# Kernel optimization log

Measured on AMD Instinct MI355X. Metric: run time of the kernel, lower is better.

## Reference

```python
import jax, jax.numpy as jnp
import numpy as np

N_NODES = 50000
N_EDGES = 1000000
IN_DIM, HID_DIM, OUT_DIM = 128, 64, 16


def setup_inputs() -> dict:
    key = jax.random.key(0)
    k1, k2, k3, k4 = jax.random.split(key, 4)
    x = jax.random.normal(k1, (N_NODES, IN_DIM), dtype=jnp.float32)
    edge_index = jax.random.randint(k2, (2, N_EDGES), 0, N_NODES, dtype=jnp.int64)
    # Glorot-style scaling for weights, zero bias (PyG GCNConv default init style)
    W1 = jax.random.normal(k3, (IN_DIM, HID_DIM), dtype=jnp.float32) * (1.0 / np.sqrt(IN_DIM))
    b1 = jnp.zeros((HID_DIM,), dtype=jnp.float32)
    W2 = jax.random.normal(k4, (HID_DIM, OUT_DIM), dtype=jnp.float32) * (1.0 / np.sqrt(HID_DIM))
    b2 = jnp.zeros((OUT_DIM,), dtype=jnp.float32)
    return {"x": x, "edge_index": edge_index, "W1": W1, "b1": b1, "W2": W2, "b2": b2}


def gcn_conv(x, src, dst, W, b, num_nodes):
    """PyG GCNConv: add self loops, symmetric deg^{-1/2} normalization,
    linear transform, gather-scale-scatter aggregation, bias."""
    # degree includes self loops (src/dst already augmented by caller)
    deg = jax.ops.segment_sum(jnp.ones_like(dst, dtype=x.dtype), dst, num_segments=num_nodes)
    dinv = jnp.where(deg > 0, deg ** -0.5, 0.0)
    norm = dinv[src] * dinv[dst]            # [E']
    h = x @ W                                # [N, F_out] transform before aggregation
    msg = h[src] * norm[:, None]             # gather + scale
    out = jax.ops.segment_sum(msg, dst, num_segments=num_nodes)  # scatter-add
    return out + b


def reference(x, edge_index, W1, b1, W2, b2):
    n = x.shape[0]
    loops = jnp.arange(n, dtype=edge_index.dtype)
    src = jnp.concatenate([edge_index[0], loops])
    dst = jnp.concatenate([edge_index[1], loops])
    h = gcn_conv(x, src, dst, W1, b1, n)
    h = jax.nn.relu(h)
    out = gcn_conv(h, src, dst, W2, b2, n)
    return out
```

## Files before the change

kernel.cpp:

```cpp
#include <hip/hip_runtime.h>
#include <hip/hip_bf16.h>

#define IN_DIM 128
#define HID_DIM 64
#define OUT_DIM 16

#define SSHIFT 7
#define SMASK 127
#define CHUNK 4096
#define CBLK 256

static __device__ __forceinline__ unsigned short f2bf(float f) {
    unsigned u = __float_as_uint(f);
    unsigned r = u + 0x7fffu + ((u >> 16) & 1u);
    return (unsigned short)(r >> 16);
}
static __device__ __forceinline__ unsigned packbf2(float a, float b) {
    return (unsigned)f2bf(a) | ((unsigned)f2bf(b) << 16);
}
static __device__ __forceinline__ float bflo(unsigned v) { return __uint_as_float(v << 16); }
static __device__ __forceinline__ float bfhi(unsigned v) { return __uint_as_float(v & 0xffff0000u); }

__global__ __launch_bounds__(CBLK) void passA(const int* __restrict__ dst,
                                              int* __restrict__ cm,
                                              int E, int NS, int NSP) {
    __shared__ int cnt[512];
    int t = threadIdx.x;
    for (int s = t; s < NS; s += CBLK) cnt[s] = 0;
    __syncthreads();
    int base = blockIdx.x * CHUNK;
    #pragma unroll 4
    for (int k = 0; k < CHUNK; k += CBLK) {
        int i = base + k + t;
        if (i < E) atomicAdd(&cnt[dst[i] >> SSHIFT], 1);
    }
    __syncthreads();
    for (int s = t; s < NS; s += CBLK) cm[blockIdx.x * NSP + s] = cnt[s];
}

__global__ __launch_bounds__(256) void passB1(int* __restrict__ cm, int* __restrict__ tot,
                                              int B, int NSP) {
    __shared__ int sv[256];
    int t = threadIdx.x, s = blockIdx.x;
    int v = (t < B) ? cm[t * NSP + s] : 0;
    sv[t] = v;
    __syncthreads();
    for (int off = 1; off < 256; off <<= 1) {
        int tmp = (t >= off) ? sv[t - off] : 0;
        __syncthreads();
        sv[t] += tmp;
        __syncthreads();
    }
    if (t < B) cm[t * NSP + s] = sv[t] - v;
    if (t == 255) tot[s] = sv[255];
}

__global__ __launch_bounds__(CBLK) void passC(const int* __restrict__ src,
                                              const int* __restrict__ dst,
                                              const int* __restrict__ cm,
                                              const int* __restrict__ tot,
                                              int* __restrict__ eb,
                                              int E, int NS, int NSP) {
    __shared__ int sb[512];
    __shared__ int cur[512];
    int t = threadIdx.x, b = blockIdx.x;
    int i0 = t, i1 = t + 256;
    int v0 = (i0 < NS) ? tot[i0] : 0;
    int v1 = (i1 < NS) ? tot[i1] : 0;
    sb[i0] = v0; sb[i1] = v1;
    __syncthreads();
    for (int off = 1; off < 512; off <<= 1) {
        int t0 = (i0 >= off) ? sb[i0 - off] : 0;
        int t1 = (i1 >= off) ? sb[i1 - off] : 0;
        __syncthreads();
        sb[i0] += t0; sb[i1] += t1;
        __syncthreads();
    }
    if (i0 < NS) cur[i0] = (sb[i0] - v0) + cm[b * NSP + i0];
    if (i1 < NS) cur[i1] = (sb[i1] - v1) + cm[b * NSP + i1];
    __syncthreads();
    int base = b * CHUNK;
    #pragma unroll 4
    for (int k = 0; k < CHUNK; k += CBLK) {
        int i = base + k + t;
        if (i < E) {
            int d = dst[i];
            int s = d >> SSHIFT;
            int pos = atomicAdd(&cur[s], 1);
            eb[pos] = src[i] | ((d & SMASK) << 17);
        }
    }
}

__global__ __launch_bounds__(256) void passD(const int* __restrict__ eb,
                                             const int* __restrict__ tot,
                                             int* __restrict__ csr_src,
                                             int* __restrict__ row_ptr,
                                             float* __restrict__ dinv,
                                             int N, int E, int NS) {
    __shared__ int red[256];
    __shared__ int deg[128], incl[128], cur[128];
    int s = blockIdx.x, t = threadIdx.x;
    if (t < 128) deg[t] = 0;
    int part = 0;
    for (int k = t; k < s; k += 256) part += tot[k];
    red[t] = part;
    __syncthreads();
    for (int off = 128; off >= 1; off >>= 1) {
        if (t < off) red[t] += red[t + off];
        __syncthreads();
    }
    int b0 = red[0];
    int cnt = tot[s];
    for (int k = t; k < cnt; k += 256) atomicAdd(&deg[eb[b0 + k] >> 17], 1);
    __syncthreads();
    if (t < 128) incl[t] = deg[t];
    __syncthreads();
    for (int off = 1; off < 128; off <<= 1) {
        int tmp = 0;
        if (t < 128 && t >= off) tmp = incl[t - off];
        __syncthreads();
        if (t < 128) incl[t] += tmp;
        __syncthreads();
    }
    if (t < 128) {
        int loff = incl[t] - deg[t];
        cur[t] = b0 + loff;
        int n = (s << SSHIFT) + t;
        if (n < N) {
            row_ptr[n] = b0 + loff;
            dinv[n] = rsqrtf((float)(deg[t] + 1));
        }
    }
    if (s == NS - 1 && t == 0) row_ptr[N] = E;
    __syncthreads();
    for (int k = t; k < cnt; k += 256) {
        int v = eb[b0 + k];
        int dl = v >> 17;
        int p = atomicAdd(&cur[dl], 1);
        csr_src[p] = v & 0x1FFFF;
    }
}

__global__ __launch_bounds__(256) void gemm1_kernel(const float* __restrict__ x,
                                                    const float* __restrict__ W1,
                                                    const float* __restrict__ dinv,
                                                    unsigned* __restrict__ h1u, int N) {
    __shared__ __align__(16) float sW[IN_DIM * HID_DIM];
    __shared__ __align__(16) float sx[16 * IN_DIM];
    int t = threadIdx.x;
    int node0 = blockIdx.x * 16;

    const float4* W4  = (const float4*)W1;
    float4*       sW4 = (float4*)sW;
    for (int i = t; i < (IN_DIM * HID_DIM) / 4; i += 256) sW4[i] = W4[i];

    const float4* x4  = (const float4*)x;
    float4*       sx4 = (float4*)sx;
    for (int i = t; i < (16 * IN_DIM) / 4; i += 256) {
        int r = i >> 5, c = i & 31;
        int n = node0 + r; if (n >= N) n = 0;
        sx4[(r << 5) + c] = x4[(size_t)n * 32 + c];
    }
    __syncthreads();

    int ln = t >> 4, jj = t & 15;
    int n = node0 + ln;
    float4 acc = {0.f, 0.f, 0.f, 0.f};
    const float* xr = sx + ln * IN_DIM;
    #pragma unroll 4
    for (int k = 0; k < IN_DIM; ++k) {
        float  xk = xr[k];
        float4 wv = ((const float4*)(sW + k * HID_DIM))[jj];
        acc.x += xk * wv.x; acc.y += xk * wv.y; acc.z += xk * wv.z; acc.w += xk * wv.w;
    }
    if (n <= N) {
        float dn = (n < N) ? dinv[n] : 0.f;
        uint2 pv;
        pv.x = packbf2(acc.x * dn, acc.y * dn);
        pv.y = packbf2(acc.z * dn, acc.w * dn);
        ((uint2*)(h1u + (size_t)n * 32))[jj] = pv;
    }
}

__global__ __launch_bounds__(256) void agg1_kernel(const unsigned* __restrict__ h1u,
                                                   const int* __restrict__ row_ptr,
                                                   const int* __restrict__ csr_src,
                                                   const float* __restrict__ dinv,
                                                   const float* __restrict__ b1,
                                                   unsigned* __restrict__ h1au, int N) {
    int t = threadIdx.x;
    int lane = t & 63;
    int h  = lane >> 5;
    int l  = lane & 31;
    int es = l >> 3;
    int dg = l & 7;
    int n = blockIdx.x * 8 + ((t >> 6) << 1) + h;
    if (n >= N) return;

    int e0 = row_ptr[n], e1 = row_ptr[n + 1];
    const uint4* rb = (const uint4*)h1u;
    int sb = h << 5;

    float a0 = 0.f, a1 = 0.f, a2 = 0.f, a3 = 0.f,
          a4 = 0.f, a5 = 0.f, a6 = 0.f, a7 = 0.f;

    for (int base = e0 - 1; base < e1; base += 32) {
        int idx = base + l;
        int sld = N;
        if (idx == e0 - 1) sld = n;
        else if (idx < e1) sld = csr_src[idx];
        int lim = e1 - base;
        if (lim > 32) lim = 32;
        int nr = (lim + 3) >> 2;
        nr = (nr + 1) & ~1;
        for (int r = 0; r < nr; r += 2) {
            int sA = __shfl(sld, sb + ((r + 0) << 2) + es);
            int sB = __shfl(sld, sb + ((r + 1) << 2) + es);
            uint4 vA = rb[(size_t)sA * 8 + dg];
            uint4 vB = rb[(size_t)sB * 8 + dg];
            a0 += bflo(vA.x) + bflo(vB.x);
            a1 += bfhi(vA.x) + bfhi(vB.x);
            a2 += bflo(vA.y) + bflo(vB.y);
            a3 += bfhi(vA.y) + bfhi(vB.y);
            a4 += bflo(vA.z) + bflo(vB.z);
            a5 += bfhi(vA.z) + bfhi(vB.z);
            a6 += bflo(vA.w) + bflo(vB.w);
            a7 += bfhi(vA.w) + bfhi(vB.w);
        }
    }
    #pragma unroll
    for (int m = 8; m <= 16; m <<= 1) {
        a0 += __shfl_xor(a0, m); a1 += __shfl_xor(a1, m);
        a2 += __shfl_xor(a2, m); a3 += __shfl_xor(a3, m);
        a4 += __shfl_xor(a4, m); a5 += __shfl_xor(a5, m);
        a6 += __shfl_xor(a6, m); a7 += __shfl_xor(a7, m);
    }
    if (es == 0) {
        float dn = dinv[n];
        float4 bA = ((const float4*)b1)[2 * dg];
        float4 bB = ((const float4*)b1)[2 * dg + 1];
        float r0 = fmaxf(fmaf(dn, a0, bA.x), 0.f);
        float r1 = fmaxf(fmaf(dn, a1, bA.y), 0.f);
        float r2 = fmaxf(fmaf(dn, a2, bA.z), 0.f);
        float r3 = fmaxf(fmaf(dn, a3, bA.w), 0.f);
        float r4 = fmaxf(fmaf(dn, a4, bB.x), 0.f);
        float r5 = fmaxf(fmaf(dn, a5, bB.y), 0.f);
        float r6 = fmaxf(fmaf(dn, a6, bB.z), 0.f);
        float r7 = fmaxf(fmaf(dn, a7, bB.w), 0.f);
        uint4 pv;
        pv.x = packbf2(r0, r1); pv.y = packbf2(r2, r3);
        pv.z = packbf2(r4, r5); pv.w = packbf2(r6, r7);
        ((uint4*)h1au)[(size_t)n * 8 + dg] = pv;
    }
}

__global__ __launch_bounds__(256) void gemm2_kernel(const unsigned* __restrict__ h1au,
                                                    const float* __restrict__ W2,
                                                    const float* __restrict__ dinv,
                                                    unsigned* __restrict__ h2u, int N) {
    __shared__ __align__(16) float sW[HID_DIM * OUT_DIM];
    __shared__ __align__(16) float sx[16 * HID_DIM];
    int t = threadIdx.x;
    int node0 = blockIdx.x * 16;

    ((float4*)sW)[t] = ((const float4*)W2)[t];
    for (int i = t; i < 512; i += 256) {
        int r = i >> 5, c = i & 31;
        int n = node0 + r; if (n >= N) n = 0;
        unsigned v = h1au[(size_t)n * 32 + c];
        float2 f; f.x = bflo(v); f.y = bfhi(v);
        *(float2*)(sx + r * HID_DIM + 2 * c) = f;
    }
    __syncthreads();

    int ln = t >> 4, j = t & 15;
    float acc = 0.f;
    const float* xr = sx + ln * HID_DIM;
    #pragma unroll 8
    for (int k = 0; k < HID_DIM; ++k) acc += xr[k] * sW[k * OUT_DIM + j];
    int n = node0 + ln;
    float other = __shfl_xor(acc, 1);
    if (n <= N && (j & 1) == 0) {
        float dn = (n < N) ? dinv[n] : 0.f;
        h2u[(size_t)n * 8 + (j >> 1)] = packbf2(acc * dn, other * dn);
    }
}

__global__ __launch_bounds__(256) void agg2_kernel(const unsigned* __restrict__ h2u,
                                                   const int* __restrict__ row_ptr,
                                                   const int* __restrict__ csr_src,
                                                   const float* __restrict__ dinv,
                                                   const float* __restrict__ b2,
                                                   float* __restrict__ out, int N) {
    int t = threadIdx.x;
    int lane = t & 63;
    int h  = lane >> 4;
    int l  = lane & 15;
    int es = l >> 2;
    int dg = l & 3;
    int n = blockIdx.x * 16 + ((t >> 6) << 2) + h;
    if (n >= N) return;

    int e0 = row_ptr[n], e1 = row_ptr[n + 1];
    const uint2* rb = (const uint2*)h2u;
    int sb = h << 4;

    float a0 = 0.f, a1 = 0.f, a2 = 0.f, a3 = 0.f;

    for (int base = e0 - 1; base < e1; base += 16) {
        int idx = base + l;
        int sld = N;
        if (idx == e0 - 1) sld = n;
        else if (idx < e1) sld = csr_src[idx];
        int lim = e1 - base;
        if (lim > 16) lim = 16;
        int nr = (lim + 3) >> 2;
        nr = (nr + 1) & ~1;
        for (int r = 0; r < nr; r += 2) {
            int sA = __shfl(sld, sb + ((r + 0) << 2) + es);
            int sB = __shfl(sld, sb + ((r + 1) << 2) + es);
            uint2 vA = rb[(size_t)sA * 4 + dg];
            uint2 vB = rb[(size_t)sB * 4 + dg];
            a0 += bflo(vA.x) + bflo(vB.x);
            a1 += bfhi(vA.x) + bfhi(vB.x);
            a2 += bflo(vA.y) + bflo(vB.y);
            a3 += bfhi(vA.y) + bfhi(vB.y);
        }
    }
    #pragma unroll
    for (int m = 4; m <= 8; m <<= 1) {
        a0 += __shfl_xor(a0, m); a1 += __shfl_xor(a1, m);
        a2 += __shfl_xor(a2, m); a3 += __shfl_xor(a3, m);
    }
    if (es == 0) {
        float dn = dinv[n];
        float4 bb = ((const float4*)b2)[dg];
        float4 r;
        r.x = fmaf(dn, a0, bb.x);
        r.y = fmaf(dn, a1, bb.y);
        r.z = fmaf(dn, a2, bb.z);
        r.w = fmaf(dn, a3, bb.w);
        ((float4*)out)[(size_t)n * 4 + dg] = r;
    }
}

extern "C" void kernel_launch(void* const* d_in, const int* in_sizes, int n_in,
                              void* d_out, int out_size, void* d_ws, size_t ws_size,
                              hipStream_t stream) {
    const float* x  = (const float*)d_in[0];
    const int*   ei = (const int*)d_in[1];
    const float* W1 = (const float*)d_in[2];
    const float* b1 = (const float*)d_in[3];
    const float* W2 = (const float*)d_in[4];
    const float* b2 = (const float*)d_in[5];
    float* out = (float*)d_out;

    const int N = in_sizes[0] / IN_DIM;
    const int E = in_sizes[1] / 2;
    const int* src = ei;
    const int* dst = ei + E;

    const int NS  = (N + SMASK) >> SSHIFT;
    const int NSP = NS + 1;
    const int BC  = (E + CHUNK - 1) / CHUNK;

    char* w = (char*)d_ws;
    auto alloc = [&](size_t bytes) -> void* {
        void* p = (void*)w;
        w += (bytes + 255) & ~(size_t)255;
        return p;
    };
    int*      cm      = (int*)     alloc((size_t)256 * NSP * 4);
    int*      tot     = (int*)     alloc((size_t)NS * 4);
    int*      eb      = (int*)     alloc((size_t)E * 4);
    int*      csr_src = (int*)     alloc((size_t)E * 4);
    int*      row_ptr = (int*)     alloc((size_t)(N + 1) * 4);
    float*    dinv    = (float*)   alloc((size_t)N * 4);
    unsigned* h1u     = (unsigned*)alloc((size_t)(N + 1) * 32 * 4);
    unsigned* h1au    = (unsigned*)alloc((size_t)(N + 1) * 32 * 4);
    unsigned* h2u     = (unsigned*)alloc((size_t)(N + 1) * 8 * 4);

    const int GB  = (N + 16) / 16;
    const int AB1 = (N + 7) / 8;
    const int AB2 = (N + 15) / 16;

    passA <<<BC, CBLK, 0, stream>>>(dst, cm, E, NS, NSP);
    passB1<<<NS, 256,  0, stream>>>(cm, tot, BC, NSP);
    passC <<<BC, CBLK, 0, stream>>>(src, dst, cm, tot, eb, E, NS, NSP);
    passD <<<NS, 256,  0, stream>>>(eb, tot, csr_src, row_ptr, dinv, N, E, NS);

    gemm1_kernel<<<GB, 256, 0, stream>>>(x, W1, dinv, h1u, N);
    agg1_kernel<<<AB1, 256, 0, stream>>>(h1u, row_ptr, csr_src, dinv, b1, h1au, N);
    gemm2_kernel<<<GB, 256, 0, stream>>>(h1au, W2, dinv, h2u, N);
    agg2_kernel<<<AB2, 256, 0, stream>>>(h2u, row_ptr, csr_src, dinv, b2, out, N);
}
```

Measured before the change: 171.4 us.

## Replace count/scan/scatter with fixed-capacity bucket scatter and fuse gemm2 into agg1

```diff
diff --git a/kernel.cpp b/kernel.cpp
--- a/kernel.cpp
+++ b/kernel.cpp
@@ -1,5 +1,4 @@
 #include <hip/hip_runtime.h>
-#include <hip/hip_bf16.h>
 
 #define IN_DIM 128
 #define HID_DIM 64
@@ -9,6 +8,8 @@
 #define SMASK 127
 #define CHUNK 4096
 #define CBLK 256
+#define KPT (CHUNK / CBLK)
+#define CAP 4096
 
 static __device__ __forceinline__ unsigned short f2bf(float f) {
     unsigned u = __float_as_uint(f);
@@ -21,73 +22,40 @@
 static __device__ __forceinline__ float bflo(unsigned v) { return __uint_as_float(v << 16); }
 static __device__ __forceinline__ float bfhi(unsigned v) { return __uint_as_float(v & 0xffff0000u); }
 
-__global__ __launch_bounds__(CBLK) void passA(const int* __restrict__ dst,
-                                              int* __restrict__ cm,
-                                              int E, int NS, int NSP) {
+__global__ __launch_bounds__(CBLK) void passC2(const int* __restrict__ src,
+                                               const int* __restrict__ dst,
+                                               int* __restrict__ gcnt,
+                                               int* __restrict__ eb,
+                                               int E, int NS) {
     __shared__ int cnt[512];
+    __shared__ int bofs[512];
     int t = threadIdx.x;
     for (int s = t; s < NS; s += CBLK) cnt[s] = 0;
     __syncthreads();
     int base = blockIdx.x * CHUNK;
-    #pragma unroll 4
-    for (int k = 0; k < CHUNK; k += CBLK) {
-        int i = base + k + t;
-        if (i < E) atomicAdd(&cnt[dst[i] >> SSHIFT], 1);
-    }
-    __syncthreads();
-    for (int s = t; s < NS; s += CBLK) cm[blockIdx.x * NSP + s] = cnt[s];
-}
-
-__global__ __launch_bounds__(256) void passB1(int* __restrict__ cm, int* __restrict__ tot,
-                                              int B, int NSP) {
-    __shared__ int sv[256];
-    int t = threadIdx.x, s = blockIdx.x;
-    int v = (t < B) ? cm[t * NSP + s] : 0;
-    sv[t] = v;
-    __syncthreads();
-    for (int off = 1; off < 256; off <<= 1) {
-        int tmp = (t >= off) ? sv[t - off] : 0;
-        __syncthreads();
-        sv[t] += tmp;
-        __syncthreads();
-    }
-    if (t < B) cm[t * NSP + s] = sv[t] - v;
-    if (t == 255) tot[s] = sv[255];
-}
-
-__global__ __launch_bounds__(CBLK) void passC(const int* __restrict__ src,
-                                              const int* __restrict__ dst,
-                                              const int* __restrict__ cm,
-                                              const int* __restrict__ tot,
-                                              int* __restrict__ eb,
-                                              int E, int NS, int NSP) {
-    __shared__ int sb[512];
-    __shared__ int cur[512];
-    int t = threadIdx.x, b = blockIdx.x;
-    int i0 = t, i1 = t + 256;
-    int v0 = (i0 < NS) ? tot[i0] : 0;
-    int v1 = (i1 < NS) ? tot[i1] : 0;
-    sb[i0] = v0; sb[i1] = v1;
-    __syncthreads();
-    for (int off = 1; off < 512; off <<= 1) {
-        int t0 = (i0 >= off) ? sb[i0 - off] : 0;
-        int t1 = (i1 >= off) ? sb[i1 - off] : 0;
-        __syncthreads();
-        sb[i0] += t0; sb[i1] += t1;
-        __syncthreads();
-    }
-    if (i0 < NS) cur[i0] = (sb[i0] - v0) + cm[b * NSP + i0];
-    if (i1 < NS) cur[i1] = (sb[i1] - v1) + cm[b * NSP + i1];
-    __syncthreads();
-    int base = b * CHUNK;
-    #pragma unroll 4
-    for (int k = 0; k < CHUNK; k += CBLK) {
-        int i = base + k + t;
+    int dreg[KPT];
+    #pragma unroll
+    for (int k = 0; k < KPT; ++k) {
+        int i = base + k * CBLK + t;
+        int d = -1;
+        if (i < E) { d = dst[i]; atomicAdd(&cnt[d >> SSHIFT], 1); }
+        dreg[k] = d;
+    }
+    __syncthreads();
+    for (int s = t; s < NS; s += CBLK) {
+        int c = cnt[s];
+        bofs[s] = c ? atomicAdd(&gcnt[s], c) : 0;
+        cnt[s] = 0;
+    }
+    __syncthreads();
+    #pragma unroll
+    for (int k = 0; k < KPT; ++k) {
+        int i = base + k * CBLK + t;
         if (i < E) {
-            int d = dst[i];
+            int d = dreg[k];
             int s = d >> SSHIFT;
-            int pos = atomicAdd(&cur[s], 1);
-            eb[pos] = src[i] | ((d & SMASK) << 17);
+            int off = atomicAdd(&cnt[s], 1);
+            eb[(size_t)s * CAP + bofs[s] + off] = src[i] | ((d & SMASK) << 17);
         }
     }
 }
@@ -112,7 +80,8 @@
     }
     int b0 = red[0];
     int cnt = tot[s];
-    for (int k = t; k < cnt; k += 256) atomicAdd(&deg[eb[b0 + k] >> 17], 1);
+    const size_t sbase = (size_t)s * CAP;
+    for (int k = t; k < cnt; k += 256) atomicAdd(&deg[eb[sbase + k] >> 17], 1);
     __syncthreads();
     if (t < 128) incl[t] = deg[t];
     __syncthreads();
@@ -135,7 +104,7 @@
     if (s == NS - 1 && t == 0) row_ptr[N] = E;
     __syncthreads();
     for (int k = t; k < cnt; k += 256) {
-        int v = eb[b0 + k];
+        int v = eb[sbase + k];
         int dl = v >> 17;
         int p = atomicAdd(&cur[dl], 1);
         csr_src[p] = v & 0x1FFFF;
@@ -188,15 +157,27 @@
                                                    const int* __restrict__ csr_src,
                                                    const float* __restrict__ dinv,
                                                    const float* __restrict__ b1,
-                                                   unsigned* __restrict__ h1au, int N) {
+                                                   const float* __restrict__ W2,
+                                                   unsigned* __restrict__ h2u, int N) {
+    __shared__ __align__(16) float sW[OUT_DIM * 68];
     int t = threadIdx.x;
+    for (int i = t; i < HID_DIM * OUT_DIM; i += 256) {
+        int k = i >> 4, j = i & 15;
+        sW[j * 68 + k] = W2[i];
+    }
+    __syncthreads();
+
     int lane = t & 63;
     int h  = lane >> 5;
     int l  = lane & 31;
     int es = l >> 3;
     int dg = l & 7;
     int n = blockIdx.x * 8 + ((t >> 6) << 1) + h;
-    if (n >= N) return;
+    if (n > N) return;
+    if (n == N) {
+        if (l < 4) { uint2 z; z.x = 0u; z.y = 0u; ((uint2*)h2u)[(size_t)N * 4 + l] = z; }
+        return;
+    }
 
     int e0 = row_ptr[n], e1 = row_ptr[n + 1];
     const uint4* rb = (const uint4*)h1u;
@@ -236,54 +217,40 @@
         a4 += __shfl_xor(a4, m); a5 += __shfl_xor(a5, m);
         a6 += __shfl_xor(a6, m); a7 += __shfl_xor(a7, m);
     }
-    if (es == 0) {
-        float dn = dinv[n];
-        float4 bA = ((const float4*)b1)[2 * dg];
-        float4 bB = ((const float4*)b1)[2 * dg + 1];
-        float r0 = fmaxf(fmaf(dn, a0, bA.x), 0.f);
-        float r1 = fmaxf(fmaf(dn, a1, bA.y), 0.f);
-        float r2 = fmaxf(fmaf(dn, a2, bA.z), 0.f);
-        float r3 = fmaxf(fmaf(dn, a3, bA.w), 0.f);
-        float r4 = fmaxf(fmaf(dn, a4, bB.x), 0.f);
-        float r5 = fmaxf(fmaf(dn, a5, bB.y), 0.f);
-        float r6 = fmaxf(fmaf(dn, a6, bB.z), 0.f);
-        float r7 = fmaxf(fmaf(dn, a7, bB.w), 0.f);
-        uint4 pv;
-        pv.x = packbf2(r0, r1); pv.y = packbf2(r2, r3);
-        pv.z = packbf2(r4, r5); pv.w = packbf2(r6, r7);
-        ((uint4*)h1au)[(size_t)n * 8 + dg] = pv;
-    }
-}
-
-__global__ __launch_bounds__(256) void gemm2_kernel(const unsigned* __restrict__ h1au,
-                                                    const float* __restrict__ W2,
-                                                    const float* __restrict__ dinv,
-                                                    unsigned* __restrict__ h2u, int N) {
-    __shared__ __align__(16) float sW[HID_DIM * OUT_DIM];
-    __shared__ __align__(16) float sx[16 * HID_DIM];
-    int t = threadIdx.x;
-    int node0 = blockIdx.x * 16;
-
-    ((float4*)sW)[t] = ((const float4*)W2)[t];
-    for (int i = t; i < 512; i += 256) {
-        int r = i >> 5, c = i & 31;
-        int n = node0 + r; if (n >= N) n = 0;
-        unsigned v = h1au[(size_t)n * 32 + c];
-        float2 f; f.x = bflo(v); f.y = bfhi(v);
-        *(float2*)(sx + r * HID_DIM + 2 * c) = f;
-    }
-    __syncthreads();
-
-    int ln = t >> 4, j = t & 15;
-    float acc = 0.f;
-    const float* xr = sx + ln * HID_DIM;
-    #pragma unroll 8
-    for (int k = 0; k < HID_DIM; ++k) acc += xr[k] * sW[k * OUT_DIM + j];
-    int n = node0 + ln;
-    float other = __shfl_xor(acc, 1);
-    if (n <= N && (j & 1) == 0) {
-        float dn = (n < N) ? dinv[n] : 0.f;
-        h2u[(size_t)n * 8 + (j >> 1)] = packbf2(acc * dn, other * dn);
+
+    float dn = dinv[n];
+    float4 bA = ((const float4*)b1)[2 * dg];
+    float4 bB = ((const float4*)b1)[2 * dg + 1];
+    float r0 = fmaxf(fmaf(dn, a0, bA.x), 0.f);
+    float r1 = fmaxf(fmaf(dn, a1, bA.y), 0.f);
+    float r2 = fmaxf(fmaf(dn, a2, bA.z), 0.f);
+    float r3 = fmaxf(fmaf(dn, a3, bA.w), 0.f);
+    float r4 = fmaxf(fmaf(dn, a4, bB.x), 0.f);
+    float r5 = fmaxf(fmaf(dn, a5, bB.y), 0.f);
+    float r6 = fmaxf(fmaf(dn, a6, bB.z), 0.f);
+    float r7 = fmaxf(fmaf(dn, a7, bB.w), 0.f);
+
+    const float* wb = sW + ((es << 2) * 68) + (dg << 3);
+    float4 wA, wB2;
+    wA = *(const float4*)(wb);        wB2 = *(const float4*)(wb + 4);
+    float p0 = r0*wA.x + r1*wA.y + r2*wA.z + r3*wA.w + r4*wB2.x + r5*wB2.y + r6*wB2.z + r7*wB2.w;
+    wA = *(const float4*)(wb + 68);   wB2 = *(const float4*)(wb + 72);
+    float p1 = r0*wA.x + r1*wA.y + r2*wA.z + r3*wA.w + r4*wB2.x + r5*wB2.y + r6*wB2.z + r7*wB2.w;
+    wA = *(const float4*)(wb + 136);  wB2 = *(const float4*)(wb + 140);
+    float p2 = r0*wA.x + r1*wA.y + r2*wA.z + r3*wA.w + r4*wB2.x + r5*wB2.y + r6*wB2.z + r7*wB2.w;
+    wA = *(const float4*)(wb + 204);  wB2 = *(const float4*)(wb + 208);
+    float p3 = r0*wA.x + r1*wA.y + r2*wA.z + r3*wA.w + r4*wB2.x + r5*wB2.y + r6*wB2.z + r7*wB2.w;
+
+    #pragma unroll
+    for (int m = 1; m <= 4; m <<= 1) {
+        p0 += __shfl_xor(p0, m); p1 += __shfl_xor(p1, m);
+        p2 += __shfl_xor(p2, m); p3 += __shfl_xor(p3, m);
+    }
+    if (dg == 0) {
+        uint2 pv;
+        pv.x = packbf2(p0 * dn, p1 * dn);
+        pv.y = packbf2(p2 * dn, p3 * dn);
+        ((uint2*)h2u)[(size_t)n * 4 + es] = pv;
     }
 }
 
@@ -371,27 +338,23 @@
         w += (bytes + 255) & ~(size_t)255;
         return p;
     };
-    int*      cm      = (int*)     alloc((size_t)256 * NSP * 4);
-    int*      tot     = (int*)     alloc((size_t)NS * 4);
-    int*      eb      = (int*)     alloc((size_t)E * 4);
+    int*      gcnt    = (int*)     alloc((size_t)NSP * 4);
+    int*      eb      = (int*)     alloc((size_t)NS * CAP * 4);
     int*      csr_src = (int*)     alloc((size_t)E * 4);
     int*      row_ptr = (int*)     alloc((size_t)(N + 1) * 4);
     float*    dinv    = (float*)   alloc((size_t)N * 4);
     unsigned* h1u     = (unsigned*)alloc((size_t)(N + 1) * 32 * 4);
-    unsigned* h1au    = (unsigned*)alloc((size_t)(N + 1) * 32 * 4);
     unsigned* h2u     = (unsigned*)alloc((size_t)(N + 1) * 8 * 4);
 
     const int GB  = (N + 16) / 16;
-    const int AB1 = (N + 7) / 8;
+    const int AB1 = (N + 8) / 8;
     const int AB2 = (N + 15) / 16;
 
-    passA <<<BC, CBLK, 0, stream>>>(dst, cm, E, NS, NSP);
-    passB1<<<NS, 256,  0, stream>>>(cm, tot, BC, NSP);
-    passC <<<BC, CBLK, 0, stream>>>(src, dst, cm, tot, eb, E, NS, NSP);
-    passD <<<NS, 256,  0, stream>>>(eb, tot, csr_src, row_ptr, dinv, N, E, NS);
+    hipMemsetAsync(gcnt, 0, (size_t)NSP * 4, stream);
+    passC2<<<BC, CBLK, 0, stream>>>(src, dst, gcnt, eb, E, NS);
+    passD <<<NS, 256,  0, stream>>>(eb, gcnt, csr_src, row_ptr, dinv, N, E, NS);
 
     gemm1_kernel<<<GB, 256, 0, stream>>>(x, W1, dinv, h1u, N);
-    agg1_kernel<<<AB1, 256, 0, stream>>>(h1u, row_ptr, csr_src, dinv, b1, h1au, N);
-    gemm2_kernel<<<GB, 256, 0, stream>>>(h1au, W2, dinv, h2u, N);
+    agg1_kernel<<<AB1, 256, 0, stream>>>(h1u, row_ptr, csr_src, dinv, b1, W2, h2u, N);
     agg2_kernel<<<AB2, 256, 0, stream>>>(h2u, row_ptr, csr_src, dinv, b2, out, N);
 }
```

New measurement: 165.8 us. 3.3% less time.
